# Optimization experiments

Measured on AMD Instinct MI355X. Metric: run time of the kernel, lower is better.

The kernel has to match this reference:

```python
import jax, jax.numpy as jnp
import numpy as np

N = 12500      # nodes
E = 200000     # edges (avg degree 16)
IN = 32        # inp_dim
OUT = 32       # out_dim
ATTN = 32      # attn_rel_emb_dim
R = 200        # num_rels
NB = 50        # num_bases


def setup_inputs() -> dict:
    key = jax.random.key(0)
    ks = jax.random.split(key, 10)
    node_feat = jax.random.normal(ks[0], (N, IN), jnp.float32)
    total_edge = jax.random.randint(ks[1], (2, E), 0, N)
    total_target_relation = jax.random.normal(ks[2], (E, ATTN), jnp.float32)
    total_relation_embed = jax.random.normal(ks[3], (E, ATTN), jnp.float32)
    total_relation = jax.random.randint(ks[4], (E,), 0, R)
    # learned parameters (xavier-ish scale)
    weight = jax.random.normal(ks[5], (NB, IN, OUT), jnp.float32) * 0.1
    w_comp = jax.random.normal(ks[6], (R, NB), jnp.float32) * 0.1
    self_loop_weight = jax.random.normal(ks[7], (IN, OUT), jnp.float32) * 0.1
    A_w = jax.random.normal(ks[8], (IN, 2 * IN + 2 * ATTN), jnp.float32) * 0.1
    A_b = jnp.zeros((IN,), jnp.float32)
    B_w = jax.random.normal(ks[9], (1, IN), jnp.float32) * 0.1
    B_b = jnp.zeros((1,), jnp.float32)
    return {
        'node_feat': node_feat,
        'total_target_relation': total_target_relation,
        'total_relation_embed': total_relation_embed,
        'weight': weight,
        'w_comp': w_comp,
        'self_loop_weight': self_loop_weight,
        'A_w': A_w,
        'A_b': A_b,
        'B_w': B_w,
        'B_b': B_b,
        'total_edge': total_edge,
        'total_relation': total_relation,
    }


def reference(node_feat, total_target_relation, total_relation_embed,
              weight, w_comp, self_loop_weight, A_w, A_b, B_w, B_b,
              total_edge, total_relation):
    # basis decomposition: per-relation weight [R, IN, OUT]
    rel_w = jnp.einsum('rb,bio->rio', w_comp, weight)
    src = node_feat[total_edge[0]]            # [E, IN]
    tgt = node_feat[total_edge[1]]            # [E, IN]
    # per-edge relation-specific transform (bmm in torch)
    msg = jnp.einsum('ei,eio->eo', src, rel_w[total_relation])  # [E, OUT]
    curr = tgt @ self_loop_weight             # [E, OUT]
    # attention MLP: sigmoid(B(relu(A(concat))))
    e = jnp.concatenate([src, tgt, total_relation_embed, total_target_relation], axis=1)
    h = jax.nn.relu(e @ A_w.T + A_b)
    a = jax.nn.sigmoid(h @ B_w.T + B_b)       # [E, 1]
    curr = curr + msg * a
    # gnn_spmm(e2n_sp, curr): scatter-add edge messages to target nodes
    out = jax.ops.segment_sum(curr, total_edge[1], num_segments=node_feat.shape[0])
    return out  # [N, OUT]
```

## Files before the change

kernel.cpp:

```cpp
#include <hip/hip_runtime.h>

#define N_NODES 12500
#define N_EDGES 200000
#define DIM 32
#define N_REL 200
#define N_BASES 50

#define OUT_ELEMS   (N_NODES * DIM)
#define ZERO_BLOCKS ((OUT_ELEMS + 1023) / 1024)

#define AWBF_OFF  (N_REL * 1024 * 4)
#define SLWT_OFF  (AWBF_OFF + 32 * 128 * 2)

typedef __attribute__((ext_vector_type(8))) short short8;
typedef __attribute__((ext_vector_type(4))) float f32x4;

__device__ __forceinline__ unsigned short f2bf(float x) {
    union { float f; unsigned u; } v; v.f = x;
    unsigned r = (v.u + 0x7FFFu + ((v.u >> 16) & 1u)) >> 16;
    return (unsigned short)r;
}

__device__ __forceinline__ short8 cvt8(float4 a, float4 b) {
    short8 r;
    r[0] = (short)f2bf(a.x); r[1] = (short)f2bf(a.y);
    r[2] = (short)f2bf(a.z); r[3] = (short)f2bf(a.w);
    r[4] = (short)f2bf(b.x); r[5] = (short)f2bf(b.y);
    r[6] = (short)f2bf(b.z); r[7] = (short)f2bf(b.w);
    return r;
}

#define MFMA(A, B, C) __builtin_amdgcn_mfma_f32_16x16x32_bf16(A, B, C, 0, 0, 0)

__global__ __launch_bounds__(256) void prep_kernel(
    const float* __restrict__ weight,
    const float* __restrict__ w_comp,
    const float* __restrict__ Aw,
    const float* __restrict__ slw,
    float* __restrict__ rel_w,
    unsigned short* __restrict__ aw_bf,
    unsigned short* __restrict__ slwT_bf,
    float* __restrict__ out)
{
    int b = blockIdx.x, tid = threadIdx.x;
    if (b < N_REL) {
        __shared__ float wc[N_BASES];
        if (tid < N_BASES) wc[tid] = w_comp[b * N_BASES + tid];
        __syncthreads();
        for (int t = 0; t < 4; t++) {
            int idx = tid + t * 256;
            float sum = 0.f;
            #pragma unroll 10
            for (int bb = 0; bb < N_BASES; bb++)
                sum = fmaf(wc[bb], weight[bb * 1024 + idx], sum);
            rel_w[b * 1024 + idx] = sum;
        }
    } else if (b < N_REL + ZERO_BLOCKS) {
        int base = (b - N_REL) * 1024 + tid * 4;
        if (base + 3 < OUT_ELEMS)
            *(float4*)(out + base) = make_float4(0.f, 0.f, 0.f, 0.f);
        else
            for (int k = 0; k < 4; k++)
                if (base + k < OUT_ELEMS) out[base + k] = 0.f;
    } else {
        for (int x = tid; x < 32 * 128; x += 256) aw_bf[x] = f2bf(Aw[x]);
        for (int x = tid; x < 32 * 32; x += 256) {
            int i = x >> 5, j = x & 31;
            slwT_bf[j * 32 + i] = f2bf(slw[x]);
        }
    }
}

__global__ __launch_bounds__(256) void edge_kernel(
    const float* __restrict__ node_feat,
    const float* __restrict__ ttr,
    const float* __restrict__ tre,
    const float* __restrict__ Ab,
    const float* __restrict__ Bw,
    const float* __restrict__ Bb,
    const int*  __restrict__ edge0,
    const int*  __restrict__ edge1,
    const int*  __restrict__ rel,
    const float* __restrict__ rel_w,
    const unsigned short* __restrict__ aw_bf,
    const unsigned short* __restrict__ slwT_bf,
    float* __restrict__ out)
{
    __shared__ float msgL[4 * 16 * 36];

    int tid  = threadIdx.x;
    int wave = tid >> 6;
    int lane = tid & 63;
    int m = lane & 15;
    int q = lane >> 4;
    int base = blockIdx.x * 64 + wave * 16;

    int s_ld = 0, t_ld = 0, r_ld = 0;
    if (lane < 16) {
        int eid = base + lane;
        int s = edge0[eid]; s_ld = s < 0 ? 0 : (s >= N_NODES ? N_NODES - 1 : s);
        int t = edge1[eid]; t_ld = t < 0 ? 0 : (t >= N_NODES ? N_NODES - 1 : t);
        int r = rel[eid];   r_ld = r < 0 ? 0 : (r >= N_REL   ? N_REL   - 1 : r);
    }
    int s_m = __shfl(s_ld, m, 64);
    int t_m = __shfl(t_ld, m, 64);
    int eid_m = base + m;

    const float* sp = node_feat + s_m * DIM + q * 8;
    float4 sv0 = *(const float4*)sp, sv1 = *(const float4*)(sp + 4);
    const float* tp = node_feat + t_m * DIM + q * 8;
    float4 tv0 = *(const float4*)tp, tv1 = *(const float4*)(tp + 4);
    const float* rp = tre + eid_m * DIM + q * 8;
    float4 rv0 = *(const float4*)rp, rv1 = *(const float4*)(rp + 4);
    const float* qp = ttr + eid_m * DIM + q * 8;
    float4 qv0 = *(const float4*)qp, qv1 = *(const float4*)(qp + 4);

    short8 fsrc = cvt8(sv0, sv1);
    short8 ftgt = cvt8(tv0, tv1);
    short8 fre  = cvt8(rv0, rv1);
    short8 ftr  = cvt8(qv0, qv1);

    short8 bA[4][2], bS[2];
    #pragma unroll
    for (int hh = 0; hh < 2; hh++) {
        #pragma unroll
        for (int c = 0; c < 4; c++)
            bA[c][hh] = *(const short8*)(aw_bf + (16 * hh + m) * 128 + 32 * c + 8 * q);
        bS[hh] = *(const short8*)(slwT_bf + (16 * hh + m) * 32 + 8 * q);
    }

    float ab0 = Ab[m], ab1 = Ab[16 + m];
    f32x4 hacc0 = {ab0, ab0, ab0, ab0};
    f32x4 hacc1 = {ab1, ab1, ab1, ab1};
    f32x4 cacc0 = {0.f, 0.f, 0.f, 0.f};
    f32x4 cacc1 = {0.f, 0.f, 0.f, 0.f};

    hacc0 = MFMA(fsrc, bA[0][0], hacc0);  hacc1 = MFMA(fsrc, bA[0][1], hacc1);
    hacc0 = MFMA(ftgt, bA[1][0], hacc0);  hacc1 = MFMA(ftgt, bA[1][1], hacc1);
    hacc0 = MFMA(fre,  bA[2][0], hacc0);  hacc1 = MFMA(fre,  bA[2][1], hacc1);
    hacc0 = MFMA(ftr,  bA[3][0], hacc0);  hacc1 = MFMA(ftr,  bA[3][1], hacc1);
    cacc0 = MFMA(ftgt, bS[0], cacc0);     cacc1 = MFMA(ftgt, bS[1], cacc1);

    int e_loc = lane >> 2;
    int cq    = lane & 3;
    int r_e = __shfl(r_ld, e_loc, 64);
    const float* rw = rel_w + r_e * 1024 + cq * 8;
    float sf[8] = {sv0.x, sv0.y, sv0.z, sv0.w, sv1.x, sv1.y, sv1.z, sv1.w};
    float msg[8] = {0.f, 0.f, 0.f, 0.f, 0.f, 0.f, 0.f, 0.f};
    #pragma unroll
    for (int k = 0; k < 32; k++) {
        float s_k = __shfl(sf[k & 7], e_loc + 16 * (k >> 3), 64);
        float4 w0 = *(const float4*)(rw + k * 32);
        float4 w1 = *(const float4*)(rw + k * 32 + 4);
        msg[0] = fmaf(s_k, w0.x, msg[0]); msg[1] = fmaf(s_k, w0.y, msg[1]);
        msg[2] = fmaf(s_k, w0.z, msg[2]); msg[3] = fmaf(s_k, w0.w, msg[3]);
        msg[4] = fmaf(s_k, w1.x, msg[4]); msg[5] = fmaf(s_k, w1.y, msg[5]);
        msg[6] = fmaf(s_k, w1.z, msg[6]); msg[7] = fmaf(s_k, w1.w, msg[7]);
    }

    float* ml = msgL + wave * (16 * 36);
    *(float4*)(ml + e_loc * 36 + cq * 8)     = make_float4(msg[0], msg[1], msg[2], msg[3]);
    *(float4*)(ml + e_loc * 36 + cq * 8 + 4) = make_float4(msg[4], msg[5], msg[6], msg[7]);
    __syncthreads();

    float bw0 = Bw[m], bw1 = Bw[16 + m], Bb0 = Bb[0];
    float av[4];
    #pragma unroll
    for (int v = 0; v < 4; v++) {
        float p = fmaxf(hacc0[v], 0.f) * bw0 + fmaxf(hacc1[v], 0.f) * bw1;
        p += __shfl_xor(p, 1, 16);
        p += __shfl_xor(p, 2, 16);
        p += __shfl_xor(p, 4, 16);
        p += __shfl_xor(p, 8, 16);
        av[v] = 1.f / (1.f + __expf(-(p + Bb0)));
    }
    #pragma unroll
    for (int v = 0; v < 4; v++) {
        int row = 4 * q + v;
        int tv = __shfl(t_ld, row, 64);
        float m0 = ml[row * 36 + m];
        float m1 = ml[row * 36 + 16 + m];
        atomicAdd(&out[tv * DIM + m],      cacc0[v] + m0 * av[v]);
        atomicAdd(&out[tv * DIM + 16 + m], cacc1[v] + m1 * av[v]);
    }
}

extern "C" void kernel_launch(void* const* d_in, const int* in_sizes, int n_in,
                              void* d_out, int out_size, void* d_ws, size_t ws_size,
                              hipStream_t stream) {
    const float* node_feat = (const float*)d_in[0];
    const float* ttr       = (const float*)d_in[1];
    const float* tre       = (const float*)d_in[2];
    const float* weight    = (const float*)d_in[3];
    const float* w_comp    = (const float*)d_in[4];
    const float* slw       = (const float*)d_in[5];
    const float* Aw        = (const float*)d_in[6];
    const float* Ab        = (const float*)d_in[7];
    const float* Bw        = (const float*)d_in[8];
    const float* Bb        = (const float*)d_in[9];
    const int*  total_edge = (const int*)d_in[10];
    const int*  rel        = (const int*)d_in[11];
    const int*  edge0 = total_edge;
    const int*  edge1 = total_edge + N_EDGES;

    float* rel_w = (float*)d_ws;
    unsigned short* aw_bf   = (unsigned short*)((char*)d_ws + AWBF_OFF);
    unsigned short* slwT_bf = (unsigned short*)((char*)d_ws + SLWT_OFF);
    float* out = (float*)d_out;

    prep_kernel<<<N_REL + ZERO_BLOCKS + 1, 256, 0, stream>>>(
        weight, w_comp, Aw, slw, rel_w, aw_bf, slwT_bf, out);

    edge_kernel<<<N_EDGES / 64, 256, 0, stream>>>(
        node_feat, ttr, tre, Ab, Bw, Bb,
        edge0, edge1, rel, rel_w, aw_bf, slwT_bf, out);
}
```

Baseline: 169.7 us.

## Store per-relation weights as bf16 and drop block barrier in edge kernel

Precomputes the basis-combined relation weights in bf16 instead of fp32, halving the bytes gathered per edge in the message matvec, and vectorises the prep combination loop with float4 loads. Also removes the __syncthreads between the per-wave LDS message write and read, since each wave only touches its own slice. Trades weight precision for memory traffic and relies on intra-wave LDS ordering without an explicit barrier.

```diff
diff --git a/kernel.cpp b/kernel.cpp
--- a/kernel.cpp
+++ b/kernel.cpp
@@ -9,11 +9,12 @@
 #define OUT_ELEMS   (N_NODES * DIM)
 #define ZERO_BLOCKS ((OUT_ELEMS + 1023) / 1024)
 
-#define AWBF_OFF  (N_REL * 1024 * 4)
+#define AWBF_OFF  (N_REL * 1024 * 2)
 #define SLWT_OFF  (AWBF_OFF + 32 * 128 * 2)
 
 typedef __attribute__((ext_vector_type(8))) short short8;
 typedef __attribute__((ext_vector_type(4))) float f32x4;
+typedef __attribute__((ext_vector_type(4))) unsigned short us4;
 
 __device__ __forceinline__ unsigned short f2bf(float x) {
     union { float f; unsigned u; } v; v.f = x;
@@ -37,7 +38,7 @@
     const float* __restrict__ w_comp,
     const float* __restrict__ Aw,
     const float* __restrict__ slw,
-    float* __restrict__ rel_w,
+    unsigned short* __restrict__ relw_bf,
     unsigned short* __restrict__ aw_bf,
     unsigned short* __restrict__ slwT_bf,
     float* __restrict__ out)
@@ -47,14 +48,19 @@
         __shared__ float wc[N_BASES];
         if (tid < N_BASES) wc[tid] = w_comp[b * N_BASES + tid];
         __syncthreads();
-        for (int t = 0; t < 4; t++) {
-            int idx = tid + t * 256;
-            float sum = 0.f;
-            #pragma unroll 10
-            for (int bb = 0; bb < N_BASES; bb++)
-                sum = fmaf(wc[bb], weight[bb * 1024 + idx], sum);
-            rel_w[b * 1024 + idx] = sum;
+        const float* wp = weight + tid * 4;
+        float4 acc = make_float4(0.f, 0.f, 0.f, 0.f);
+        #pragma unroll 10
+        for (int bb = 0; bb < N_BASES; bb++) {
+            float4 w = *(const float4*)(wp + bb * 1024);
+            float c = wc[bb];
+            acc.x = fmaf(c, w.x, acc.x); acc.y = fmaf(c, w.y, acc.y);
+            acc.z = fmaf(c, w.z, acc.z); acc.w = fmaf(c, w.w, acc.w);
         }
+        us4 o;
+        o[0] = f2bf(acc.x); o[1] = f2bf(acc.y);
+        o[2] = f2bf(acc.z); o[3] = f2bf(acc.w);
+        *(us4*)(relw_bf + b * 1024 + tid * 4) = o;
     } else if (b < N_REL + ZERO_BLOCKS) {
         int base = (b - N_REL) * 1024 + tid * 4;
         if (base + 3 < OUT_ELEMS)
@@ -81,7 +87,7 @@
     const int*  __restrict__ edge0,
     const int*  __restrict__ edge1,
     const int*  __restrict__ rel,
-    const float* __restrict__ rel_w,
+    const unsigned short* __restrict__ relw_bf,
     const unsigned short* __restrict__ aw_bf,
     const unsigned short* __restrict__ slwT_bf,
     float* __restrict__ out)
@@ -144,24 +150,26 @@
     int e_loc = lane >> 2;
     int cq    = lane & 3;
     int r_e = __shfl(r_ld, e_loc, 64);
-    const float* rw = rel_w + r_e * 1024 + cq * 8;
+    const unsigned short* rwb = relw_bf + r_e * 1024 + cq * 8;
     float sf[8] = {sv0.x, sv0.y, sv0.z, sv0.w, sv1.x, sv1.y, sv1.z, sv1.w};
     float msg[8] = {0.f, 0.f, 0.f, 0.f, 0.f, 0.f, 0.f, 0.f};
     #pragma unroll
     for (int k = 0; k < 32; k++) {
         float s_k = __shfl(sf[k & 7], e_loc + 16 * (k >> 3), 64);
-        float4 w0 = *(const float4*)(rw + k * 32);
-        float4 w1 = *(const float4*)(rw + k * 32 + 4);
-        msg[0] = fmaf(s_k, w0.x, msg[0]); msg[1] = fmaf(s_k, w0.y, msg[1]);
-        msg[2] = fmaf(s_k, w0.z, msg[2]); msg[3] = fmaf(s_k, w0.w, msg[3]);
-        msg[4] = fmaf(s_k, w1.x, msg[4]); msg[5] = fmaf(s_k, w1.y, msg[5]);
-        msg[6] = fmaf(s_k, w1.z, msg[6]); msg[7] = fmaf(s_k, w1.w, msg[7]);
+        union { short8 s; unsigned u[4]; } W;
+        W.s = *(const short8*)(rwb + k * 32);
+        #pragma unroll
+        for (int p = 0; p < 4; p++) {
+            float lo = __uint_as_float(W.u[p] << 16);
+            float hi = __uint_as_float(W.u[p] & 0xffff0000u);
+            msg[2 * p]     = fmaf(s_k, lo, msg[2 * p]);
+            msg[2 * p + 1] = fmaf(s_k, hi, msg[2 * p + 1]);
+        }
     }
 
     float* ml = msgL + wave * (16 * 36);
     *(float4*)(ml + e_loc * 36 + cq * 8)     = make_float4(msg[0], msg[1], msg[2], msg[3]);
     *(float4*)(ml + e_loc * 36 + cq * 8 + 4) = make_float4(msg[4], msg[5], msg[6], msg[7]);
-    __syncthreads();
 
     float bw0 = Bw[m], bw1 = Bw[16 + m], Bb0 = Bb[0];
     float av[4];
@@ -203,15 +211,15 @@
     const int*  edge0 = total_edge;
     const int*  edge1 = total_edge + N_EDGES;
 
-    float* rel_w = (float*)d_ws;
+    unsigned short* relw_bf = (unsigned short*)d_ws;
     unsigned short* aw_bf   = (unsigned short*)((char*)d_ws + AWBF_OFF);
     unsigned short* slwT_bf = (unsigned short*)((char*)d_ws + SLWT_OFF);
     float* out = (float*)d_out;
 
     prep_kernel<<<N_REL + ZERO_BLOCKS + 1, 256, 0, stream>>>(
-        weight, w_comp, Aw, slw, rel_w, aw_bf, slwT_bf, out);
+        weight, w_comp, Aw, slw, relw_bf, aw_bf, slwT_bf, out);
 
     edge_kernel<<<N_EDGES / 64, 256, 0, stream>>>(
         node_feat, ttr, tre, Ab, Bw, Bb,
-        edge0, edge1, rel, rel_w, aw_bf, slwT_bf, out);
-}
+        edge0, edge1, rel, relw_bf, aw_bf, slwT_bf, out);
+}
```

Result: faster. 152.8 us (-10.0%).
